# Kernel optimization log

Measured on AMD Instinct MI355X. Metric: run time of the kernel, lower is better.

The kernel has to match this reference:

```python
import jax, jax.numpy as jnp
import numpy as np


def setup_inputs() -> dict:
    key = jax.random.key(0)
    k1, _ = jax.random.split(key)
    N, H, CH, T = 4, 8, 64, 2048
    qkv = jax.random.normal(k1, (N, H * 3 * CH, T), dtype=jnp.float32)
    rescale = jnp.ones((1,), dtype=jnp.float32)
    return {"qkv": qkv, "rescale": rescale, "n_heads": H}


def reference(qkv, rescale, n_heads):
    bs, width, length = qkv.shape
    ch = width // (3 * n_heads)
    # [N, H*3*C, T] -> [N*H, 3*C, T] -> three [N*H, C, T]
    qkv_h = qkv.reshape(bs * n_heads, 3 * ch, length)
    q, k, v = qkv_h[:, :ch], qkv_h[:, ch:2 * ch], qkv_h[:, 2 * ch:]
    scale = 1.0 / jnp.sqrt(jnp.sqrt(jnp.float32(ch)))
    # scores: [B*H, T, S]
    weight = jnp.einsum('bct,bcs->bts', q * scale, k * scale)
    weight = jax.nn.softmax(weight.astype(jnp.float32) * rescale[0], axis=-1).astype(qkv.dtype)
    a = jnp.einsum('bts,bcs->bct', weight, v)  # [B*H, C, T]
    return a.reshape(bs, n_heads * ch, length)
```

## Files before the change

### kernel.cpp

```cpp
#include <hip/hip_runtime.h>

typedef _Float16 half8 __attribute__((ext_vector_type(8)));
typedef _Float16 half4 __attribute__((ext_vector_type(4)));
typedef float    floatx4 __attribute__((ext_vector_type(4)));

#define T_LEN 2048
#define CH 64
#define BH 32
#define QTILE 64
#define LDP 72
#define FRAG_BH 131072

__global__ __launch_bounds__(256, 2)
void prep_kernel(const float* __restrict__ qkv, const float* __restrict__ rescale,
                 _Float16* __restrict__ ws)
{
    __shared__ _Float16 Qs[64][LDP];
    __shared__ _Float16 Ks[64][LDP];
    __shared__ _Float16 Vs[64][LDP];

    const int tid  = threadIdx.x;
    const int bh   = blockIdx.y;
    const int tile = blockIdx.x;
    const int x0   = tile * 64;

    const float qscale = 0.125f * 1.4426950408889634f * rescale[0];

    const float* qp = qkv + (size_t)(bh >> 3) * (1536 * T_LEN)
                          + (size_t)(bh & 7) * (192 * T_LEN);
    const float* kp = qp + 64 * T_LEN;
    const float* vp = qp + 128 * T_LEN;

    {
        const int a4 = (tid & 15) * 4;
        const int c4 = (tid >> 4) * 4;
        float4 rq[4], rk[4];
#pragma unroll
        for (int i = 0; i < 4; ++i) {
            rq[i] = *(const float4*)(qp + (size_t)(c4 + i) * T_LEN + x0 + a4);
            rk[i] = *(const float4*)(kp + (size_t)(c4 + i) * T_LEN + x0 + a4);
        }
#pragma unroll
        for (int j = 0; j < 4; ++j) {
            half4 hq, hk;
#pragma unroll
            for (int i = 0; i < 4; ++i) {
                hq[i] = (_Float16)((&rq[i].x)[j] * qscale);
                hk[i] = (_Float16)((&rk[i].x)[j]);
            }
            *(half4*)&Qs[a4 + j][c4] = hq;
            *(half4*)&Ks[a4 + j][c4] = hk;
        }
        const int s4 = (tid & 15) * 4;
        const int cv = tid >> 4;
#pragma unroll
        for (int i = 0; i < 4; ++i) {
            const int c = cv + 16 * i;
            float4 r = *(const float4*)(vp + (size_t)c * T_LEN + x0 + s4);
            half4 h; h[0]=(_Float16)r.x; h[1]=(_Float16)r.y; h[2]=(_Float16)r.z; h[3]=(_Float16)r.w;
            *(half4*)&Vs[c][s4] = h;
        }
    }
    __syncthreads();

    const int lane = tid & 63, wave = tid >> 6;
    const int l15 = lane & 15, quad = lane >> 4;
    _Float16* qf = ws;
    _Float16* kf = ws + (size_t)BH * FRAG_BH;
    _Float16* vf = ws + (size_t)2 * BH * FRAG_BH;

#pragma unroll
    for (int ks = 0; ks < 2; ++ks) {
        half8 hq = *(const half8*)&Qs[wave * 16 + l15][ks * 32 + quad * 8];
        half8 hk = *(const half8*)&Ks[wave * 16 + l15][ks * 32 + quad * 8];
        half8 hv = *(const half8*)&Vs[wave * 16 + l15][ks * 32 + quad * 8];
        const size_t gqk = (((size_t)bh * 128 + tile * 4 + wave) * 2 + ks) * 512 + lane * 8;
        *(half8*)(qf + gqk) = hq;
        *(half8*)(kf + gqk) = hk;
        *(half8*)(vf + (((size_t)bh * 32 + tile) * 8 + wave * 2 + ks) * 512 + lane * 8) = hv;
    }
}

__global__ __launch_bounds__(256, 4)
void attn_kernel(const _Float16* __restrict__ ws, float* __restrict__ out)
{
    __shared__ _Float16 Pt[4][16][LDP];

    const int tid  = threadIdx.x;
    const int wave = tid >> 6;
    const int lane = tid & 63;
    const int l15  = lane & 15;
    const int quad = lane >> 4;

    const int bh = blockIdx.y;
    const int t0 = blockIdx.x * QTILE;

    const _Float16* qf = ws;
    const _Float16* kf = ws + (size_t)BH * FRAG_BH;
    const _Float16* vf = ws + (size_t)2 * BH * FRAG_BH;
    float* op = out + (size_t)bh * (CH * T_LEN);

    half8 bq[2];
#pragma unroll
    for (int ks = 0; ks < 2; ++ks)
        bq[ks] = *(const half8*)(qf +
            (((size_t)bh * 128 + blockIdx.x * 4 + wave) * 2 + ks) * 512 + lane * 8);

    const floatx4 fzero = {0.f, 0.f, 0.f, 0.f};
    floatx4 oacc[4];
#pragma unroll
    for (int ct = 0; ct < 4; ++ct) oacc[ct] = fzero;
    floatx4 lacc = fzero;

    half8 bones;
#pragma unroll
    for (int i = 0; i < 8; ++i) bones[i] = (_Float16)1.0f;

    const _Float16* kfp = kf + (size_t)bh * FRAG_BH + lane * 8;
    const _Float16* vfp = vf + (size_t)bh * FRAG_BH + lane * 8;

    for (int st = 0; st < 32; ++st) {
        half8 ak[4][2], bv[4][2];
#pragma unroll
        for (int mt = 0; mt < 4; ++mt)
#pragma unroll
            for (int ks = 0; ks < 2; ++ks) {
                ak[mt][ks] = *(const half8*)(kfp + (size_t)(mt * 2 + ks) * 512);
                bv[mt][ks] = *(const half8*)(vfp + (size_t)(mt * 2 + ks) * 512);
            }
        kfp += 4096;
        vfp += 4096;

        floatx4 sacc[4];
#pragma unroll
        for (int mt = 0; mt < 4; ++mt) sacc[mt] = fzero;
#pragma unroll
        for (int mt = 0; mt < 4; ++mt)
#pragma unroll
            for (int ks = 0; ks < 2; ++ks)
                sacc[mt] = __builtin_amdgcn_mfma_f32_16x16x32_f16(
                    ak[mt][ks], bq[ks], sacc[mt], 0, 0, 0);

#pragma unroll
        for (int mt = 0; mt < 4; ++mt) {
            half4 ph;
#pragma unroll
            for (int r = 0; r < 4; ++r)
                ph[r] = (_Float16)__builtin_amdgcn_exp2f(sacc[mt][r]);
            *(half4*)&Pt[wave][l15][mt * 16 + quad * 4] = ph;
        }
        asm volatile("s_waitcnt lgkmcnt(0)" ::: "memory");

        half8 ap[2];
#pragma unroll
        for (int ks = 0; ks < 2; ++ks)
            ap[ks] = *(const half8*)&Pt[wave][l15][ks * 32 + quad * 8];

#pragma unroll
        for (int ks = 0; ks < 2; ++ks)
            lacc = __builtin_amdgcn_mfma_f32_16x16x32_f16(ap[ks], bones, lacc, 0, 0, 0);

#pragma unroll
        for (int ct = 0; ct < 4; ++ct)
#pragma unroll
            for (int ks = 0; ks < 2; ++ks)
                oacc[ct] = __builtin_amdgcn_mfma_f32_16x16x32_f16(
                    ap[ks], bv[ct][ks], oacc[ct], 0, 0, 0);
    }

    float linv[4];
#pragma unroll
    for (int r = 0; r < 4; ++r) linv[r] = 1.0f / lacc[r];

#pragma unroll
    for (int ct = 0; ct < 4; ++ct) {
        const int c = ct * 16 + l15;
        const int t = t0 + wave * 16 + quad * 4;
        float4 o;
#pragma unroll
        for (int r = 0; r < 4; ++r)
            (&o.x)[r] = oacc[ct][r] * linv[r];
        *(float4*)(op + (size_t)c * T_LEN + t) = o;
    }
}

extern "C" void kernel_launch(void* const* d_in, const int* in_sizes, int n_in,
                              void* d_out, int out_size, void* d_ws, size_t ws_size,
                              hipStream_t stream) {
    const float* qkv     = (const float*)d_in[0];
    const float* rescale = (const float*)d_in[1];
    float* out = (float*)d_out;
    _Float16* ws = (_Float16*)d_ws;

    prep_kernel<<<dim3(32, BH), dim3(256), 0, stream>>>(qkv, rescale, ws);
    attn_kernel<<<dim3(T_LEN / QTILE, BH), dim3(256), 0, stream>>>(ws, out);
}
```

Baseline: 159.4 us.

## Software-pipeline attention loop with 32-key steps and double-buffered P tile

Shrinks each loop step from 64 to 32 keys and restructures the attention loop so the PV and row-sum MFMAs for the previous step are issued while K fragments for the next step load and the next QK^T/exp is computed. The P tile in shared memory is double-buffered per wave, and the explicit lgkmcnt wait is removed. The goal is to overlap global loads, exp, and MFMA work and to cut register pressure. The cost is more loop iterations and reliance on wave-level ordering of the LDS write and read for correctness.

```diff
diff --git a/kernel.cpp b/kernel.cpp
--- a/kernel.cpp
+++ b/kernel.cpp
@@ -9,6 +9,7 @@
 #define BH 32
 #define QTILE 64
 #define LDP 72
+#define PTP 40
 #define FRAG_BH 131072
 
 __global__ __launch_bounds__(256, 2)
@@ -84,7 +85,7 @@
 __global__ __launch_bounds__(256, 4)
 void attn_kernel(const _Float16* __restrict__ ws, float* __restrict__ out)
 {
-    __shared__ _Float16 Pt[4][16][LDP];
+    __shared__ _Float16 Pt[4][2][16][PTP];
 
     const int tid  = threadIdx.x;
     const int wave = tid >> 6;
@@ -119,54 +120,78 @@
     const _Float16* kfp = kf + (size_t)bh * FRAG_BH + lane * 8;
     const _Float16* vfp = vf + (size_t)bh * FRAG_BH + lane * 8;
 
-    for (int st = 0; st < 32; ++st) {
-        half8 ak[4][2], bv[4][2];
-#pragma unroll
-        for (int mt = 0; mt < 4; ++mt)
-#pragma unroll
-            for (int ks = 0; ks < 2; ++ks) {
-                ak[mt][ks] = *(const half8*)(kfp + (size_t)(mt * 2 + ks) * 512);
-                bv[mt][ks] = *(const half8*)(vfp + (size_t)(mt * 2 + ks) * 512);
-            }
-        kfp += 4096;
-        vfp += 4096;
-
-        floatx4 sacc[4];
-#pragma unroll
-        for (int mt = 0; mt < 4; ++mt) sacc[mt] = fzero;
-#pragma unroll
-        for (int mt = 0; mt < 4; ++mt)
+    half8 ak[2][2], bv[4], ap;
+
+#pragma unroll
+    for (int mt = 0; mt < 2; ++mt)
+#pragma unroll
+        for (int ks = 0; ks < 2; ++ks)
+            ak[mt][ks] = *(const half8*)(kfp + (size_t)(mt * 2 + ks) * 512);
+#pragma unroll
+    for (int ct = 0; ct < 4; ++ct)
+        bv[ct] = *(const half8*)(vfp + (size_t)ct * 1024);
+    {
+        floatx4 sacc[2] = {fzero, fzero};
+#pragma unroll
+        for (int mt = 0; mt < 2; ++mt)
 #pragma unroll
             for (int ks = 0; ks < 2; ++ks)
                 sacc[mt] = __builtin_amdgcn_mfma_f32_16x16x32_f16(
                     ak[mt][ks], bq[ks], sacc[mt], 0, 0, 0);
-
-#pragma unroll
-        for (int mt = 0; mt < 4; ++mt) {
+#pragma unroll
+        for (int mt = 0; mt < 2; ++mt) {
             half4 ph;
 #pragma unroll
             for (int r = 0; r < 4; ++r)
                 ph[r] = (_Float16)__builtin_amdgcn_exp2f(sacc[mt][r]);
-            *(half4*)&Pt[wave][l15][mt * 16 + quad * 4] = ph;
-        }
-        asm volatile("s_waitcnt lgkmcnt(0)" ::: "memory");
-
-        half8 ap[2];
-#pragma unroll
-        for (int ks = 0; ks < 2; ++ks)
-            ap[ks] = *(const half8*)&Pt[wave][l15][ks * 32 + quad * 8];
-
-#pragma unroll
-        for (int ks = 0; ks < 2; ++ks)
-            lacc = __builtin_amdgcn_mfma_f32_16x16x32_f16(ap[ks], bones, lacc, 0, 0, 0);
+            *(half4*)&Pt[wave][0][l15][mt * 16 + quad * 4] = ph;
+        }
+        ap = *(const half8*)&Pt[wave][0][l15][quad * 8];
+    }
+
+#pragma unroll 2
+    for (int st = 1; st < 64; ++st) {
+        const int buf = st & 1;
+        const _Float16* kcur = kfp + (size_t)st * 2048;
+#pragma unroll
+        for (int mt = 0; mt < 2; ++mt)
+#pragma unroll
+            for (int ks = 0; ks < 2; ++ks)
+                ak[mt][ks] = *(const half8*)(kcur + (size_t)(mt * 2 + ks) * 512);
 
 #pragma unroll
         for (int ct = 0; ct < 4; ++ct)
+            oacc[ct] = __builtin_amdgcn_mfma_f32_16x16x32_f16(ap, bv[ct], oacc[ct], 0, 0, 0);
+        lacc = __builtin_amdgcn_mfma_f32_16x16x32_f16(ap, bones, lacc, 0, 0, 0);
+
+        const _Float16* vcur = vfp + (size_t)(st >> 1) * 4096 + (size_t)(st & 1) * 512;
+#pragma unroll
+        for (int ct = 0; ct < 4; ++ct)
+            bv[ct] = *(const half8*)(vcur + (size_t)ct * 1024);
+
+        floatx4 sacc[2] = {fzero, fzero};
+#pragma unroll
+        for (int mt = 0; mt < 2; ++mt)
 #pragma unroll
             for (int ks = 0; ks < 2; ++ks)
-                oacc[ct] = __builtin_amdgcn_mfma_f32_16x16x32_f16(
-                    ap[ks], bv[ct][ks], oacc[ct], 0, 0, 0);
-    }
+                sacc[mt] = __builtin_amdgcn_mfma_f32_16x16x32_f16(
+                    ak[mt][ks], bq[ks], sacc[mt], 0, 0, 0);
+
+#pragma unroll
+        for (int mt = 0; mt < 2; ++mt) {
+            half4 ph;
+#pragma unroll
+            for (int r = 0; r < 4; ++r)
+                ph[r] = (_Float16)__builtin_amdgcn_exp2f(sacc[mt][r]);
+            *(half4*)&Pt[wave][buf][l15][mt * 16 + quad * 4] = ph;
+        }
+        ap = *(const half8*)&Pt[wave][buf][l15][quad * 8];
+    }
+
+#pragma unroll
+    for (int ct = 0; ct < 4; ++ct)
+        oacc[ct] = __builtin_amdgcn_mfma_f32_16x16x32_f16(ap, bv[ct], oacc[ct], 0, 0, 0);
+    lacc = __builtin_amdgcn_mfma_f32_16x16x32_f16(ap, bones, lacc, 0, 0, 0);
 
     float linv[4];
 #pragma unroll
```

New measurement: 174.9 us. +9.8%, slower.

## Stage K tiles in LDS via async global_load_lds double buffering

Applied to the files above, without the earlier changes.

Each K tile is now loaded once per block into a double-buffered LDS array using asynchronous global-to-LDS copies. Previously all four waves fetched the same K fragments from global memory separately. The next tile's load is issued while the current tile is computed, and V is still read directly into registers. This costs a block-wide barrier every iteration and more LDS per block, which could lower occupancy. It also drops the explicit lgkmcnt wait before reading back the Pt tile and relies on the compiler to order that LDS access.

```diff
diff --git a/kernel.cpp b/kernel.cpp
--- a/kernel.cpp
+++ b/kernel.cpp
@@ -1,4 +1,5 @@
 #include <hip/hip_runtime.h>
+#include <stdint.h>
 
 typedef _Float16 half8 __attribute__((ext_vector_type(8)));
 typedef _Float16 half4 __attribute__((ext_vector_type(4)));
@@ -9,7 +10,14 @@
 #define BH 32
 #define QTILE 64
 #define LDP 72
+#define PTP 72
 #define FRAG_BH 131072
+
+__device__ __forceinline__ void load16_lds(const _Float16* g, const _Float16* l) {
+    __builtin_amdgcn_global_load_lds(
+        (const __attribute__((address_space(1))) uint32_t*)(uintptr_t)g,
+        (__attribute__((address_space(3))) uint32_t*)(uintptr_t)l, 16, 0, 0);
+}
 
 __global__ __launch_bounds__(256, 2)
 void prep_kernel(const float* __restrict__ qkv, const float* __restrict__ rescale,
@@ -84,7 +92,8 @@
 __global__ __launch_bounds__(256, 4)
 void attn_kernel(const _Float16* __restrict__ ws, float* __restrict__ out)
 {
-    __shared__ _Float16 Pt[4][16][LDP];
+    __shared__ _Float16 KL[2][4096];
+    __shared__ _Float16 Pt[4][16][PTP];
 
     const int tid  = threadIdx.x;
     const int wave = tid >> 6;
@@ -100,6 +109,9 @@
     const _Float16* vf = ws + (size_t)2 * BH * FRAG_BH;
     float* op = out + (size_t)bh * (CH * T_LEN);
 
+    const _Float16* ktile = kf + (size_t)bh * FRAG_BH;
+    const _Float16* vfp   = vf + (size_t)bh * FRAG_BH + lane * 8;
+
     half8 bq[2];
 #pragma unroll
     for (int ks = 0; ks < 2; ++ks)
@@ -116,20 +128,37 @@
 #pragma unroll
     for (int i = 0; i < 8; ++i) bones[i] = (_Float16)1.0f;
 
-    const _Float16* kfp = kf + (size_t)bh * FRAG_BH + lane * 8;
-    const _Float16* vfp = vf + (size_t)bh * FRAG_BH + lane * 8;
-
+#pragma unroll
+    for (int c = 0; c < 2; ++c)
+        load16_lds(ktile + wave * 1024 + c * 512 + lane * 8, &KL[0][wave * 1024 + c * 512]);
+    __syncthreads();
+
+#pragma unroll 1
     for (int st = 0; st < 32; ++st) {
-        half8 ak[4][2], bv[4][2];
+        const int buf = st & 1;
+
+        const _Float16* vcur = vfp + (size_t)st * 4096;
+        half8 bv[4][2];
+#pragma unroll
+        for (int ct = 0; ct < 4; ++ct)
+#pragma unroll
+            for (int ks = 0; ks < 2; ++ks)
+                bv[ct][ks] = *(const half8*)(vcur + (size_t)(ct * 2 + ks) * 512);
+
+        if (st < 31) {
+            const _Float16* kg = ktile + (size_t)(st + 1) * 4096;
+#pragma unroll
+            for (int c = 0; c < 2; ++c)
+                load16_lds(kg + wave * 1024 + c * 512 + lane * 8,
+                           &KL[buf ^ 1][wave * 1024 + c * 512]);
+        }
+
+        half8 ak[4][2];
 #pragma unroll
         for (int mt = 0; mt < 4; ++mt)
 #pragma unroll
-            for (int ks = 0; ks < 2; ++ks) {
-                ak[mt][ks] = *(const half8*)(kfp + (size_t)(mt * 2 + ks) * 512);
-                bv[mt][ks] = *(const half8*)(vfp + (size_t)(mt * 2 + ks) * 512);
-            }
-        kfp += 4096;
-        vfp += 4096;
+            for (int ks = 0; ks < 2; ++ks)
+                ak[mt][ks] = *(const half8*)&KL[buf][(mt * 2 + ks) * 512 + lane * 8];
 
         floatx4 sacc[4];
 #pragma unroll
@@ -149,7 +178,6 @@
                 ph[r] = (_Float16)__builtin_amdgcn_exp2f(sacc[mt][r]);
             *(half4*)&Pt[wave][l15][mt * 16 + quad * 4] = ph;
         }
-        asm volatile("s_waitcnt lgkmcnt(0)" ::: "memory");
 
         half8 ap[2];
 #pragma unroll
@@ -159,19 +187,19 @@
 #pragma unroll
         for (int ks = 0; ks < 2; ++ks)
             lacc = __builtin_amdgcn_mfma_f32_16x16x32_f16(ap[ks], bones, lacc, 0, 0, 0);
-
 #pragma unroll
         for (int ct = 0; ct < 4; ++ct)
 #pragma unroll
             for (int ks = 0; ks < 2; ++ks)
                 oacc[ct] = __builtin_amdgcn_mfma_f32_16x16x32_f16(
                     ap[ks], bv[ct][ks], oacc[ct], 0, 0, 0);
+
+        __syncthreads();
     }
 
     float linv[4];
 #pragma unroll
     for (int r = 0; r < 4; ++r) linv[r] = 1.0f / lacc[r];
-
 #pragma unroll
     for (int ct = 0; ct < 4; ++ct) {
         const int c = ct * 16 + l15;
```

Result: faster. 142.1 us (-10.9%).
